# Kernel tuning notes

Hardware: AMD Instinct MI355X
Metric: run time of the kernel (lower is better)

Reference implementation:

```python
import jax, jax.numpy as jnp
import numpy as np

E = 1024   # embed_dim
H = 16     # num_heads
R = 256    # rank
HD = E // H
B, S = 2, 2048


def setup_inputs() -> dict:
    key = jax.random.key(0)
    ks = jax.random.split(key, 20)
    sc = 0.02
    d = {
        'query': jax.random.normal(ks[0], (B, S, E), jnp.float32),
        'key':   jax.random.normal(ks[1], (B, S, E), jnp.float32),
        'value': jax.random.normal(ks[2], (B, S, E), jnp.float32),
    }
    names = ['q', 'k', 'v', 'o']
    i = 3
    for n in names:
        d[f'W{n}_lo'] = jax.random.normal(ks[i], (E, R), jnp.float32) * sc; i += 1
        d[f'b{n}_lo'] = jnp.zeros((R,), jnp.float32)
        d[f'W{n}_hi'] = jax.random.normal(ks[i], (R, E), jnp.float32) * sc; i += 1
        d[f'b{n}_hi'] = jnp.zeros((E,), jnp.float32)
    return d


def _lowrank(x, W_lo, b_lo, W_hi, b_hi):
    # Linear(E->R) then Linear(R->E)
    return (x @ W_lo + b_lo) @ W_hi + b_hi


def reference(query, key, value,
              Wq_lo, bq_lo, Wq_hi, bq_hi,
              Wk_lo, bk_lo, Wk_hi, bk_hi,
              Wv_lo, bv_lo, Wv_hi, bv_hi,
              Wo_lo, bo_lo, Wo_hi, bo_hi):
    b, s, _ = query.shape
    q = _lowrank(query, Wq_lo, bq_lo, Wq_hi, bq_hi)
    k = _lowrank(key,   Wk_lo, bk_lo, Wk_hi, bk_hi)
    v = _lowrank(value, Wv_lo, bv_lo, Wv_hi, bv_hi)
    # (B, S, E) -> (B, H, S, HD)
    q = q.reshape(b, s, H, HD).transpose(0, 2, 1, 3)
    k = k.reshape(b, s, H, HD).transpose(0, 2, 1, 3)
    v = v.reshape(b, s, H, HD).transpose(0, 2, 1, 3)
    scores = jnp.einsum('bhqd,bhkd->bhqk', q, k) / jnp.sqrt(jnp.float32(HD))
    attn = jax.nn.softmax(scores, axis=-1)  # dropout p=0.0 -> identity
    out = jnp.einsum('bhqk,bhkd->bhqd', attn, v)
    out = out.transpose(0, 2, 1, 3).reshape(b, s, E)
    return _lowrank(out, Wo_lo, bo_lo, Wo_hi, bo_hi)
```

## Files before the change

### kernel.cpp

```cpp
#include <hip/hip_runtime.h>

namespace {

constexpr int kE  = 1024;
constexpr int kH  = 16;
constexpr int kR  = 256;
constexpr int kHD = 64;
constexpr int kB  = 2;
constexpr int kS  = 2048;
constexpr int kM  = kB * kS;

typedef float  floatx4 __attribute__((ext_vector_type(4)));
typedef short  short8  __attribute__((ext_vector_type(8)));
typedef short  short4  __attribute__((ext_vector_type(4)));

__device__ inline short f2bf(float f) {
  union { float f; unsigned u; } x{f};
  unsigned r = x.u + 0x7FFF + ((x.u >> 16) & 1);
  return (short)(r >> 16);
}

__device__ inline void async_copy16(const void* g, void* l) {
  __builtin_amdgcn_global_load_lds(
      (const __attribute__((address_space(1))) unsigned int*)g,
      (__attribute__((address_space(3))) unsigned int*)l,
      16, 0, 0);
}

#if defined(__HIP_DEVICE_COMPILE__)
  #if __has_builtin(__builtin_amdgcn_mfma_f32_16x16x16bf16_1k)
    #define MFMA16(a, b, c) __builtin_amdgcn_mfma_f32_16x16x16bf16_1k(a, b, c, 0, 0, 0)
  #elif __has_builtin(__builtin_amdgcn_mfma_f32_16x16x16_bf16)
    #define MFMA16(a, b, c) __builtin_amdgcn_mfma_f32_16x16x16_bf16(a, b, c, 0, 0, 0)
  #else
    #error "no 16x16x16 bf16 MFMA builtin on device"
  #endif
#else
  #define MFMA16(a, b, c) (c)
#endif

struct PrepArgs { const float* src[8]; short* dst[8]; };

__global__ __launch_bounds__(256) void prep_weights(PrepArgs pa) {
  const int id = blockIdx.y;
  const bool lo = (id & 1) == 0;
  const int K = lo ? 1024 : 256;
  const int N = lo ? 256 : 1024;
  const int tiles_k = K >> 6;
  const int k0 = (blockIdx.x % tiles_k) * 64;
  const int n0 = (blockIdx.x / tiles_k) * 64;
  const float* src = pa.src[id];
  short* dst = pa.dst[id];

  __shared__ float tile[64][68];
  const int t  = threadIdx.x;
  const int c4 = (t & 15) * 4;
  const int r  = t >> 4;

#pragma unroll
  for (int i = 0; i < 4; ++i) {
    const int rk = r + i * 16;
    *(float4*)&tile[rk][c4] = *(const float4*)&src[(size_t)(k0 + rk) * N + n0 + c4];
  }
  __syncthreads();
#pragma unroll
  for (int i = 0; i < 4; ++i) {
    const int rn = r + i * 16;
    short4 o = { f2bf(tile[c4 + 0][rn]), f2bf(tile[c4 + 1][rn]),
                 f2bf(tile[c4 + 2][rn]), f2bf(tile[c4 + 3][rn]) };
    *(short4*)&dst[(size_t)(n0 + rn) * K + k0 + c4] = o;
  }
}

__global__ __launch_bounds__(256) void convert_in(
    const float* q, const float* k, const float* v,
    short* xq, short* xk, short* xv)
{
  const float* srcs[3] = {q, k, v};
  short* dsts[3] = {xq, xk, xv};
  const float* s = srcs[blockIdx.y];
  short* d = dsts[blockIdx.y];
  const size_t i = ((size_t)blockIdx.x * 256 + threadIdx.x) * 8;
  float4 a = *(const float4*)(s + i);
  float4 b = *(const float4*)(s + i + 4);
  short8 o = { f2bf(a.x), f2bf(a.y), f2bf(a.z), f2bf(a.w),
               f2bf(b.x), f2bf(b.y), f2bf(b.z), f2bf(b.w) };
  *(short8*)(d + i) = o;
}

struct GemmArgs {
  const short* A[3]; const short* Bt[3]; const float* bias[3];
  void* C[3]; float scale[3];
};

template <int N, int K, int BM, int BN, int MODE>
__global__ __launch_bounds__(256) void gemm_bf16(GemmArgs args) {
  constexpr int TILES_N = N / BN;
  constexpr int WTM = BM / 2, WTN = BN / 2;
  constexpr int FI = WTM / 16, FJ = WTN / 16;
  constexpr int AROUNDS = (BM * 64) / 4096;
  constexpr int BROUNDS = (BN * 64) / 4096;

  const int z = blockIdx.y;
  const int row0 = (blockIdx.x / TILES_N) * BM;
  const int col0 = (blockIdx.x % TILES_N) * BN;
  const short* A  = args.A[z];
  const short* Bt = args.Bt[z];
  const float* bias = args.bias[z];
  const float scale = args.scale[z];

  __shared__ short As[BM * 32];
  __shared__ short Bs[BN * 32];

  const int t    = threadIdx.x;
  const int wave = t >> 6;
  const int lane = t & 63;
  const int lq   = lane & 15;
  const int quad = lane >> 4;
  const int wm0  = (wave >> 1) * WTM;
  const int wn0  = (wave & 1) * WTN;

  const int srow = t >> 2;
  const int scol = (t & 3) * 8;

  floatx4 acc[FI][FJ] = {};

  for (int kk = 0; kk < K; kk += 32) {
#pragma unroll
    for (int r = 0; r < AROUNDS; ++r)
      async_copy16(A + (size_t)(row0 + r * 64 + srow) * K + kk + scol,
                   (char*)As + r * 4096 + wave * 1024);
#pragma unroll
    for (int r = 0; r < BROUNDS; ++r)
      async_copy16(Bt + (size_t)(col0 + r * 64 + srow) * K + kk + scol,
                   (char*)Bs + r * 4096 + wave * 1024);
    __syncthreads();

    short8 af[FI], bf[FJ];
#pragma unroll
    for (int i = 0; i < FI; ++i)
      af[i] = *(const short8*)((const char*)As + ((wm0 + i * 16 + lq) * 64 + quad * 16));
#pragma unroll
    for (int j = 0; j < FJ; ++j)
      bf[j] = *(const short8*)((const char*)Bs + ((wn0 + j * 16 + lq) * 64 + quad * 16));
#pragma unroll
    for (int i = 0; i < FI; ++i)
#pragma unroll
      for (int j = 0; j < FJ; ++j)
        acc[i][j] = __builtin_amdgcn_mfma_f32_16x16x32_bf16(af[i], bf[j], acc[i][j], 0, 0, 0);
    __syncthreads();
  }

#pragma unroll
  for (int i = 0; i < FI; ++i) {
    const int rbase = row0 + wm0 + i * 16 + quad * 4;
#pragma unroll
    for (int j = 0; j < FJ; ++j) {
      const int col = col0 + wn0 + j * 16 + lq;
      const float bj = bias[col];
      if (MODE == 2) {
        float* C = (float*)args.C[z];
#pragma unroll
        for (int r = 0; r < 4; ++r)
          C[(size_t)(rbase + r) * N + col] = (acc[i][j][r] + bj) * scale;
      } else if (MODE == 1) {
        short* C = (short*)args.C[z];
        const int h = col >> 6, d = col & 63;
        const int b = rbase >> 11, s = rbase & 2047;
        if (z == 2) {
          short4 o = { f2bf(acc[i][j][0] + bj), f2bf(acc[i][j][1] + bj),
                       f2bf(acc[i][j][2] + bj), f2bf(acc[i][j][3] + bj) };
          *(short4*)&C[((size_t)((b * 16 + h) * 64 + d)) * 2048 + s] = o;
        } else {
#pragma unroll
          for (int r = 0; r < 4; ++r)
            C[((size_t)((b * 16 + h) * 2048 + s + r)) * 64 + d] =
                f2bf((acc[i][j][r] + bj) * scale);
        }
      } else {
        short* C = (short*)args.C[z];
#pragma unroll
        for (int r = 0; r < 4; ++r)
          C[(size_t)(rbase + r) * N + col] = f2bf((acc[i][j][r] + bj) * scale);
      }
    }
  }
}

__global__ __launch_bounds__(256) void attn_mfma(
    const short* __restrict__ Qp, const short* __restrict__ Kp,
    const short* __restrict__ Vtp, short* __restrict__ O)
{
  __shared__ short Ks[64][72];
  __shared__ short Vs[64][72];

  const int t    = threadIdx.x;
  const int wave = t >> 6;
  const int lane = t & 63;
  const int lq   = lane & 15;
  const int quad = lane >> 4;

  const int q0 = blockIdx.x * 64;
  const int bh = blockIdx.y;
  const int b  = bh >> 4;
  const int h  = bh & 15;

  const short* qrow = Qp + ((size_t)bh * kS + q0 + wave * 16 + lq) * 64;
  short8 qf0 = *(const short8*)(qrow + quad * 8);
  short8 qf1 = *(const short8*)(qrow + 32 + quad * 8);

  const short* Kbase = Kp  + (size_t)bh * kS * 64;
  const short* Vbase = Vtp + (size_t)bh * 64 * kS;

  const int srow = wave * 16 + (lane >> 3);
  const int scol = (lane & 7) * 8;

  floatx4 Oacc[4] = {};
  float m = -1e30f;
  float l = 0.f;

  short8 gk0 = *(const short8*)(Kbase + (size_t)(srow) * 64 + scol);
  short8 gk1 = *(const short8*)(Kbase + (size_t)(srow + 8) * 64 + scol);
  short8 gv0 = *(const short8*)(Vbase + (size_t)srow * kS + scol);
  short8 gv1 = *(const short8*)(Vbase + (size_t)(srow + 8) * kS + scol);

  for (int kc = 0; kc < kS; kc += 64) {
    __syncthreads();
    *(short8*)&Ks[srow][scol]     = gk0;
    *(short8*)&Ks[srow + 8][scol] = gk1;
    *(short8*)&Vs[srow][scol]     = gv0;
    *(short8*)&Vs[srow + 8][scol] = gv1;
    __syncthreads();

    if (kc + 64 < kS) {
      gk0 = *(const short8*)(Kbase + (size_t)(kc + 64 + srow) * 64 + scol);
      gk1 = *(const short8*)(Kbase + (size_t)(kc + 64 + srow + 8) * 64 + scol);
      gv0 = *(const short8*)(Vbase + (size_t)srow * kS + kc + 64 + scol);
      gv1 = *(const short8*)(Vbase + (size_t)(srow + 8) * kS + kc + 64 + scol);
    }

    floatx4 Sc[4];
#pragma unroll
    for (int tt = 0; tt < 4; ++tt) {
      short8 a0 = *(const short8*)&Ks[tt * 16 + lq][quad * 8];
      short8 a1 = *(const short8*)&Ks[tt * 16 + lq][32 + quad * 8];
      floatx4 c = {};
      c = __builtin_amdgcn_mfma_f32_16x16x32_bf16(a0, qf0, c, 0, 0, 0);
      c = __builtin_amdgcn_mfma_f32_16x16x32_bf16(a1, qf1, c, 0, 0, 0);
      Sc[tt] = c;
    }

    float mc = -1e30f;
#pragma unroll
    for (int tt = 0; tt < 4; ++tt)
#pragma unroll
      for (int r = 0; r < 4; ++r) mc = fmaxf(mc, Sc[tt][r]);
    mc = fmaxf(mc, __shfl_xor(mc, 16, 64));
    mc = fmaxf(mc, __shfl_xor(mc, 32, 64));
    const float mn = fmaxf(m, mc);
    const float alpha = __expf(m - mn);
    m = mn;

    float ls = 0.f;
    short4 pf[4];
#pragma unroll
    for (int tt = 0; tt < 4; ++tt) {
      float p0 = __expf(Sc[tt][0] - m);
      float p1 = __expf(Sc[tt][1] - m);
      float p2 = __expf(Sc[tt][2] - m);
      float p3 = __expf(Sc[tt][3] - m);
      ls += (p0 + p1) + (p2 + p3);
      pf[tt] = short4{ f2bf(p0), f2bf(p1), f2bf(p2), f2bf(p3) };
    }
    l = l * alpha + ls;
#pragma unroll
    for (int dt = 0; dt < 4; ++dt)
#pragma unroll
      for (int r = 0; r < 4; ++r) Oacc[dt][r] *= alpha;

#pragma unroll
    for (int dt = 0; dt < 4; ++dt) {
#pragma unroll
      for (int tt = 0; tt < 4; ++tt) {
        short4 vf = *(const short4*)&Vs[dt * 16 + lq][tt * 16 + quad * 4];
        Oacc[dt] = MFMA16(vf, pf[tt], Oacc[dt]);
      }
    }
  }

  l += __shfl_xor(l, 16, 64);
  l += __shfl_xor(l, 32, 64);
  const float inv = 1.f / l;

  short* orow = O + ((size_t)(b * kS + q0 + wave * 16 + lq)) * kE + h * kHD;
#pragma unroll
  for (int dt = 0; dt < 4; ++dt) {
    short4 o = { f2bf(Oacc[dt][0] * inv), f2bf(Oacc[dt][1] * inv),
                 f2bf(Oacc[dt][2] * inv), f2bf(Oacc[dt][3] * inv) };
    *(short4*)&orow[dt * 16 + quad * 4] = o;
  }
}

}

extern "C" void kernel_launch(void* const* d_in, const int* in_sizes, int n_in,
                              void* d_out, int out_size, void* d_ws, size_t ws_size,
                              hipStream_t stream) {
  short* ws = (short*)d_ws;
  short* Xq  = ws;
  short* Xk  = Xq  + (size_t)kM * kE;
  short* Xv  = Xk  + (size_t)kM * kE;
  short* Tq  = Xv  + (size_t)kM * kE;
  short* Tk  = Tq  + (size_t)kM * kR;
  short* Tv  = Tk  + (size_t)kM * kR;
  short* Qh  = Tv  + (size_t)kM * kR;
  short* Kh  = Qh  + (size_t)kM * kE;
  short* Vth = Kh  + (size_t)kM * kE;
  short* Ab  = Vth + (size_t)kM * kE;
  short* To  = Ab  + (size_t)kM * kE;
  short* Wt  = To  + (size_t)kM * kR;

  short* WtArr[8];
  for (int i = 0; i < 8; ++i) WtArr[i] = Wt + (size_t)i * (kE * kR);

  PrepArgs pa;
  const int widx[8] = {3, 5, 7, 9, 11, 13, 15, 17};
  for (int i = 0; i < 8; ++i) { pa.src[i] = (const float*)d_in[widx[i]]; pa.dst[i] = WtArr[i]; }
  prep_weights<<<dim3(64, 8), dim3(256), 0, stream>>>(pa);

  convert_in<<<dim3((kM * kE) / (256 * 8), 3), dim3(256), 0, stream>>>(
      (const float*)d_in[0], (const float*)d_in[1], (const float*)d_in[2], Xq, Xk, Xv);

  {
    GemmArgs ga;
    ga.A[0] = Xq; ga.A[1] = Xk; ga.A[2] = Xv;
    ga.Bt[0] = WtArr[0]; ga.Bt[1] = WtArr[2]; ga.Bt[2] = WtArr[4];
    ga.bias[0] = (const float*)d_in[4]; ga.bias[1] = (const float*)d_in[8]; ga.bias[2] = (const float*)d_in[12];
    ga.C[0] = Tq; ga.C[1] = Tk; ga.C[2] = Tv;
    ga.scale[0] = ga.scale[1] = ga.scale[2] = 1.f;
    gemm_bf16<kR, kE, 64, 64, 0><<<dim3((kM / 64) * (kR / 64), 3), dim3(256), 0, stream>>>(ga);
  }

  {
    GemmArgs ga;
    ga.A[0] = Tq; ga.A[1] = Tk; ga.A[2] = Tv;
    ga.Bt[0] = WtArr[1]; ga.Bt[1] = WtArr[3]; ga.Bt[2] = WtArr[5];
    ga.bias[0] = (const float*)d_in[6]; ga.bias[1] = (const float*)d_in[10]; ga.bias[2] = (const float*)d_in[14];
    ga.C[0] = Qh; ga.C[1] = Kh; ga.C[2] = Vth;
    ga.scale[0] = 0.125f; ga.scale[1] = 1.f; ga.scale[2] = 1.f;
    gemm_bf16<kE, kR, 128, 128, 1><<<dim3((kM / 128) * (kE / 128), 3), dim3(256), 0, stream>>>(ga);
  }

  attn_mfma<<<dim3(kS / 64, kB * kH), dim3(256), 0, stream>>>(Qh, Kh, Vth, Ab);

  {
    GemmArgs ga;
    ga.A[0] = Ab; ga.Bt[0] = WtArr[6];
    ga.bias[0] = (const float*)d_in[16];
    ga.C[0] = To; ga.scale[0] = 1.f;
    gemm_bf16<kR, kE, 64, 64, 0><<<dim3((kM / 64) * (kR / 64), 1), dim3(256), 0, stream>>>(ga);
  }
  {
    GemmArgs ga;
    ga.A[0] = To; ga.Bt[0] = WtArr[7];
    ga.bias[0] = (const float*)d_in[18];
    ga.C[0] = d_out; ga.scale[0] = 1.f;
    gemm_bf16<kE, kR, 128, 128, 2><<<dim3((kM / 128) * (kE / 128), 1), dim3(256), 0, stream>>>(ga);
  }
}
```

Before: 266.7 us.

## Process two query tiles per wave in attention and use exp2 with lazy rescaling

Each wave in the attention kernel now handles 32 query rows (two 16-row tiles) instead of 16, so every K/V tile staged in LDS serves twice as many queries and the grid is halved. The log2(e) factor is folded into the Q projection scale so the softmax can call a native exp2. The running max is only updated and the accumulators rescaled when some score exceeds the current max by more than a threshold, and bf16 packing moves to the hardware v_cvt_pk_bf16_f32 instruction. In exchange, registers per thread roughly double, which may lower occupancy, the grid has fewer blocks, and the lazy max lets exponents grow up to 2^10 before rescaling.

Result: faster. 250.8 us (-5.9%).

```diff
diff --git a/kernel.cpp b/kernel.cpp
--- a/kernel.cpp
+++ b/kernel.cpp
@@ -13,11 +13,36 @@
 typedef float  floatx4 __attribute__((ext_vector_type(4)));
 typedef short  short8  __attribute__((ext_vector_type(8)));
 typedef short  short4  __attribute__((ext_vector_type(4)));
+typedef unsigned int uint2v __attribute__((ext_vector_type(2)));
 
 __device__ inline short f2bf(float f) {
   union { float f; unsigned u; } x{f};
   unsigned r = x.u + 0x7FFF + ((x.u >> 16) & 1);
   return (short)(r >> 16);
+}
+
+__device__ inline unsigned cvt_pk_bf16(float a, float b) {
+#if defined(__HIP_DEVICE_COMPILE__)
+  unsigned r;
+  asm("v_cvt_pk_bf16_f32 %0, %1, %2" : "=v"(r) : "v"(a), "v"(b));
+  return r;
+#else
+  return (unsigned)(unsigned short)f2bf(a) | ((unsigned)(unsigned short)f2bf(b) << 16);
+#endif
+}
+
+__device__ inline short4 pack2(unsigned a, unsigned b) {
+  union { uint2v u; short4 s; } x;
+  x.u[0] = a; x.u[1] = b;
+  return x.s;
+}
+
+__device__ inline float fexp2(float x) {
+#if defined(__HIP_DEVICE_COMPILE__) && __has_builtin(__builtin_amdgcn_exp2f)
+  return __builtin_amdgcn_exp2f(x);
+#else
+  return exp2f(x);
+#endif
 }
 
 __device__ inline void async_copy16(const void* g, void* l) {
@@ -200,14 +225,18 @@
   const int lq   = lane & 15;
   const int quad = lane >> 4;
 
-  const int q0 = blockIdx.x * 64;
+  const int q0 = blockIdx.x * 128;
   const int bh = blockIdx.y;
   const int b  = bh >> 4;
   const int h  = bh & 15;
 
-  const short* qrow = Qp + ((size_t)bh * kS + q0 + wave * 16 + lq) * 64;
-  short8 qf0 = *(const short8*)(qrow + quad * 8);
-  short8 qf1 = *(const short8*)(qrow + 32 + quad * 8);
+  short8 qf0[2], qf1[2];
+#pragma unroll
+  for (int qt = 0; qt < 2; ++qt) {
+    const short* qrow = Qp + ((size_t)bh * kS + q0 + wave * 32 + qt * 16 + lq) * 64;
+    qf0[qt] = *(const short8*)(qrow + quad * 8);
+    qf1[qt] = *(const short8*)(qrow + 32 + quad * 8);
+  }
 
   const short* Kbase = Kp  + (size_t)bh * kS * 64;
   const short* Vbase = Vtp + (size_t)bh * 64 * kS;
@@ -215,9 +244,9 @@
   const int srow = wave * 16 + (lane >> 3);
   const int scol = (lane & 7) * 8;
 
-  floatx4 Oacc[4] = {};
-  float m = -1e30f;
-  float l = 0.f;
+  floatx4 Oacc[4][2] = {};
+  float m[2] = {-1e30f, -1e30f};
+  float l[2] = {0.f, 0.f};
 
   short8 gk0 = *(const short8*)(Kbase + (size_t)(srow) * 64 + scol);
   short8 gk1 = *(const short8*)(Kbase + (size_t)(srow + 8) * 64 + scol);
@@ -239,65 +268,79 @@
       gv1 = *(const short8*)(Vbase + (size_t)(srow + 8) * kS + kc + 64 + scol);
     }
 
-    floatx4 Sc[4];
+    floatx4 Sc[4][2];
 #pragma unroll
     for (int tt = 0; tt < 4; ++tt) {
       short8 a0 = *(const short8*)&Ks[tt * 16 + lq][quad * 8];
       short8 a1 = *(const short8*)&Ks[tt * 16 + lq][32 + quad * 8];
-      floatx4 c = {};
-      c = __builtin_amdgcn_mfma_f32_16x16x32_bf16(a0, qf0, c, 0, 0, 0);
-      c = __builtin_amdgcn_mfma_f32_16x16x32_bf16(a1, qf1, c, 0, 0, 0);
-      Sc[tt] = c;
-    }
-
-    float mc = -1e30f;
-#pragma unroll
-    for (int tt = 0; tt < 4; ++tt)
-#pragma unroll
-      for (int r = 0; r < 4; ++r) mc = fmaxf(mc, Sc[tt][r]);
-    mc = fmaxf(mc, __shfl_xor(mc, 16, 64));
-    mc = fmaxf(mc, __shfl_xor(mc, 32, 64));
-    const float mn = fmaxf(m, mc);
-    const float alpha = __expf(m - mn);
-    m = mn;
-
-    float ls = 0.f;
-    short4 pf[4];
-#pragma unroll
-    for (int tt = 0; tt < 4; ++tt) {
-      float p0 = __expf(Sc[tt][0] - m);
-      float p1 = __expf(Sc[tt][1] - m);
-      float p2 = __expf(Sc[tt][2] - m);
-      float p3 = __expf(Sc[tt][3] - m);
-      ls += (p0 + p1) + (p2 + p3);
-      pf[tt] = short4{ f2bf(p0), f2bf(p1), f2bf(p2), f2bf(p3) };
-    }
-    l = l * alpha + ls;
-#pragma unroll
-    for (int dt = 0; dt < 4; ++dt)
-#pragma unroll
-      for (int r = 0; r < 4; ++r) Oacc[dt][r] *= alpha;
+#pragma unroll
+      for (int qt = 0; qt < 2; ++qt) {
+        floatx4 c = {};
+        c = __builtin_amdgcn_mfma_f32_16x16x32_bf16(a0, qf0[qt], c, 0, 0, 0);
+        c = __builtin_amdgcn_mfma_f32_16x16x32_bf16(a1, qf1[qt], c, 0, 0, 0);
+        Sc[tt][qt] = c;
+      }
+    }
+
+    short4 pf[4][2];
+#pragma unroll
+    for (int qt = 0; qt < 2; ++qt) {
+      float x0 = fmaxf(fmaxf(Sc[0][qt][0], Sc[0][qt][1]), fmaxf(Sc[0][qt][2], Sc[0][qt][3]));
+      float x1 = fmaxf(fmaxf(Sc[1][qt][0], Sc[1][qt][1]), fmaxf(Sc[1][qt][2], Sc[1][qt][3]));
+      float x2 = fmaxf(fmaxf(Sc[2][qt][0], Sc[2][qt][1]), fmaxf(Sc[2][qt][2], Sc[2][qt][3]));
+      float x3 = fmaxf(fmaxf(Sc[3][qt][0], Sc[3][qt][1]), fmaxf(Sc[3][qt][2], Sc[3][qt][3]));
+      float plane = fmaxf(fmaxf(x0, x1), fmaxf(x2, x3));
+
+      if (!__all(plane <= m[qt] + 10.f)) {
+        float mc = fmaxf(plane, __shfl_xor(plane, 16, 64));
+        mc = fmaxf(mc, __shfl_xor(mc, 32, 64));
+        const float mn = fmaxf(m[qt], mc);
+        const float a = fexp2(m[qt] - mn);
+        m[qt] = mn;
+        l[qt] *= a;
+#pragma unroll
+        for (int dt = 0; dt < 4; ++dt) Oacc[dt][qt] *= a;
+      }
+
+      float ls = 0.f;
+#pragma unroll
+      for (int tt = 0; tt < 4; ++tt) {
+        float p0 = fexp2(Sc[tt][qt][0] - m[qt]);
+        float p1 = fexp2(Sc[tt][qt][1] - m[qt]);
+        float p2 = fexp2(Sc[tt][qt][2] - m[qt]);
+        float p3 = fexp2(Sc[tt][qt][3] - m[qt]);
+        ls += (p0 + p1) + (p2 + p3);
+        pf[tt][qt] = pack2(cvt_pk_bf16(p0, p1), cvt_pk_bf16(p2, p3));
+      }
+      l[qt] += ls;
+    }
 
 #pragma unroll
     for (int dt = 0; dt < 4; ++dt) {
 #pragma unroll
       for (int tt = 0; tt < 4; ++tt) {
         short4 vf = *(const short4*)&Vs[dt * 16 + lq][tt * 16 + quad * 4];
-        Oacc[dt] = MFMA16(vf, pf[tt], Oacc[dt]);
+#pragma unroll
+        for (int qt = 0; qt < 2; ++qt)
+          Oacc[dt][qt] = MFMA16(vf, pf[tt][qt], Oacc[dt][qt]);
       }
     }
   }
 
-  l += __shfl_xor(l, 16, 64);
-  l += __shfl_xor(l, 32, 64);
-  const float inv = 1.f / l;
-
-  short* orow = O + ((size_t)(b * kS + q0 + wave * 16 + lq)) * kE + h * kHD;
-#pragma unroll
-  for (int dt = 0; dt < 4; ++dt) {
-    short4 o = { f2bf(Oacc[dt][0] * inv), f2bf(Oacc[dt][1] * inv),
-                 f2bf(Oacc[dt][2] * inv), f2bf(Oacc[dt][3] * inv) };
-    *(short4*)&orow[dt * 16 + quad * 4] = o;
+#pragma unroll
+  for (int qt = 0; qt < 2; ++qt) {
+    float lv = l[qt];
+    lv += __shfl_xor(lv, 16, 64);
+    lv += __shfl_xor(lv, 32, 64);
+    const float inv = 1.f / lv;
+
+    short* orow = O + ((size_t)(b * kS + q0 + wave * 32 + qt * 16 + lq)) * kE + h * kHD;
+#pragma unroll
+    for (int dt = 0; dt < 4; ++dt) {
+      short4 o = pack2(cvt_pk_bf16(Oacc[dt][qt][0] * inv, Oacc[dt][qt][1] * inv),
+                       cvt_pk_bf16(Oacc[dt][qt][2] * inv, Oacc[dt][qt][3] * inv));
+      *(short4*)&orow[dt * 16 + quad * 4] = o;
+    }
   }
 }
 
@@ -347,11 +390,12 @@
     ga.Bt[0] = WtArr[1]; ga.Bt[1] = WtArr[3]; ga.Bt[2] = WtArr[5];
     ga.bias[0] = (const float*)d_in[6]; ga.bias[1] = (const float*)d_in[10]; ga.bias[2] = (const float*)d_in[14];
     ga.C[0] = Qh; ga.C[1] = Kh; ga.C[2] = Vth;
-    ga.scale[0] = 0.125f; ga.scale[1] = 1.f; ga.scale[2] = 1.f;
+    ga.scale[0] = 0.125f * 1.44269504088896340736f;
+    ga.scale[1] = 1.f; ga.scale[2] = 1.f;
     gemm_bf16<kE, kR, 128, 128, 1><<<dim3((kM / 128) * (kE / 128), 3), dim3(256), 0, stream>>>(ga);
   }
 
-  attn_mfma<<<dim3(kS / 64, kB * kH), dim3(256), 0, stream>>>(Qh, Kh, Vth, Ab);
+  attn_mfma<<<dim3(kS / 128, kB * kH), dim3(256), 0, stream>>>(Qh, Kh, Vth, Ab);
 
   {
     GemmArgs ga;
```
